# Kernel tuning notes

Measured on AMD Instinct MI355X. Metric: run time of the kernel, lower is better.

Reference implementation:

```python
import jax, jax.numpy as jnp
import numpy as np

B, L, D, H, K_DELAYS = 8, 2048, 512, 8, 8
DH = D // H


def setup_inputs() -> dict:
    key = jax.random.key(0)
    ks = jax.random.split(key, 6)
    def lin_w(k):
        return 0.02 * jax.random.normal(k, (D, D), jnp.float32)
    return {
        "x_q":  jax.random.normal(ks[0], (B, L, D), jnp.float32),
        "x_kv": jax.random.normal(ks[1], (B, L, D), jnp.float32),
        "Wq": lin_w(ks[2]), "bq": jnp.zeros((D,), jnp.float32),
        "Wk": lin_w(ks[3]), "bk": jnp.zeros((D,), jnp.float32),
        "Wv": lin_w(ks[4]), "bv": jnp.zeros((D,), jnp.float32),
        "Wo": lin_w(ks[5]), "bo": jnp.zeros((D,), jnp.float32),
    }


def reference(x_q, x_kv, Wq, bq, Wk, bk, Wv, bv, Wo, bo):
    Bx, Lx, Dx = x_q.shape

    def proj(x, W, b):  # torch Linear: x @ W.T + b, then split heads -> [B,H,L,dh]
        return (x @ W.T + b).reshape(Bx, Lx, H, DH).transpose(0, 2, 1, 3)

    q = proj(x_q, Wq, bq)
    k = proj(x_kv, Wk, bk)
    v = proj(x_kv, Wv, bv)

    # FFT-based autocorrelation over the time axis (axis=2)
    qz = q - q.mean(axis=2, keepdims=True)
    kz = k - k.mean(axis=2, keepdims=True)
    Qf = jnp.fft.rfft(qz, axis=2)
    Kf = jnp.fft.rfft(kz, axis=2)
    corr = jnp.fft.irfft(Qf * jnp.conj(Kf), n=Lx, axis=2).mean(axis=-1)  # [B,H,L]
    # torch expands corr to [B,H,Lq,Lk] then means over Lq -> identical to corr
    score = corr

    K = min(K_DELAYS, Lx)
    vals, idx = jax.lax.top_k(score, K)                    # [B,H,K]
    w = vals / (vals.sum(axis=-1, keepdims=True) + 1e-12)
    w = jax.lax.stop_gradient(w)                           # .detach() in torch

    # circular shift by -delay == gather at (t + delay) mod L
    t = jnp.arange(Lx)
    pos = (t[None, None, None, :] + idx[..., None]) % Lx   # [B,H,K,L]
    v_sh = jnp.take_along_axis(v[:, :, None, :, :], pos[..., None], axis=3)  # [B,H,K,L,dh]
    out = jnp.einsum('bhk,bhkld->bhld', w, v_sh)           # weighted sum over delays

    out = out.transpose(0, 2, 1, 3).reshape(Bx, Lx, Dx)
    return out @ Wo.T + bo
```

## Files before the change

kernel.cpp:

```cpp
#include <hip/hip_runtime.h>
#include <math.h>

#define BB 8
#define LL 2048
#define DD 512
#define HH 8
#define DHH 64
#define KD 8
#define MM (BB*LL)

typedef _Float16 f16x2 __attribute__((ext_vector_type(2)));
typedef _Float16 f16x4 __attribute__((ext_vector_type(4)));
typedef _Float16 f16x8 __attribute__((ext_vector_type(8)));
typedef float    f32x4 __attribute__((ext_vector_type(4)));

__device__ inline void cvt8(const float* __restrict__ s, _Float16* hp, _Float16* lp) {
    const float4 a = *(const float4*)s;
    const float4 b = *(const float4*)(s + 4);
    const float v[8] = {a.x, a.y, a.z, a.w, b.x, b.y, b.z, b.w};
    f16x8 hi, lo;
#pragma unroll
    for (int j = 0; j < 8; j++) {
        const _Float16 h = (_Float16)v[j];
        hi[j] = h;
        lo[j] = (_Float16)((v[j] - (float)h) * 512.0f);
    }
    *(f16x8*)hp = hi;
    if (lp) *(f16x8*)lp = lo;
}

__global__ __launch_bounds__(256) void prep_w(const float* __restrict__ Wq, const float* __restrict__ Wk,
                                              const float* __restrict__ Wv, const float* __restrict__ Wo,
                                              _Float16* __restrict__ Wq_h, _Float16* __restrict__ Wq_l,
                                              _Float16* __restrict__ Wk_h, _Float16* __restrict__ Wk_l,
                                              _Float16* __restrict__ Wv_h, _Float16* __restrict__ Wo_h) {
    const int g = blockIdx.x * 256 + threadIdx.x;
    const int which = g >> 15;
    const size_t idx = (size_t)(g & 32767) * 8;
    if (which == 0)      cvt8(Wq + idx, Wq_h + idx, Wq_l + idx);
    else if (which == 1) cvt8(Wk + idx, Wk_h + idx, Wk_l + idx);
    else if (which == 2) cvt8(Wv + idx, Wv_h + idx, nullptr);
    else                 cvt8(Wo + idx, Wo_h + idx, nullptr);
}

__device__ __forceinline__ void stage16(const _Float16* g, const _Float16* l) {
    __builtin_amdgcn_global_load_lds(
        (const __attribute__((address_space(1))) void*)g,
        (__attribute__((address_space(3))) void*)l,
        16, 0, 0);
}

template<int NPROD, int MODE, int AF32, int BK>
__device__ __forceinline__ void gemm_body(const float* __restrict__ A32,
                                          const _Float16* __restrict__ Ag,
                                          const _Float16* __restrict__ Al_g,
                                          const _Float16* __restrict__ Bg,
                                          const _Float16* __restrict__ Bl_g,
                                          const float* __restrict__ bias,
                                          void* __restrict__ Cv,
                                          _Float16* lds, int l0) {
    constexpr int CPR  = BK / 8;
    constexpr int NST  = BK / 16;
    constexpr int SH   = (BK == 32) ? 2 : 3;
    constexpr int PLN  = 128 * BK;

#define SWZR(R) ((BK == 32) ? (((R) >> 1) & 3) : ((R) & 7))
#define ASWZ(R, g) ((size_t)(R) * BK + (size_t)((((g) ^ SWZR(R))) * 8))

    _Float16* Ah = lds;
    _Float16* Bh = lds + PLN;
    _Float16* Al = (NPROD == 3) ? lds + 2 * PLN : lds;
    _Float16* Bl = (NPROD == 3) ? lds + 3 * PLN : lds;

    const int t  = threadIdx.x;
    const int m0 = (((l0 >> 5) << 3) | (l0 & 7)) * 128;
    const int n0 = ((l0 >> 3) & 3) * 128;

    const int wv   = t >> 6;
    const int lane = t & 63;
    const int wm   = (wv >> 1) * 64;
    const int wn   = (wv & 1) * 64;
    const int lm   = lane & 15;
    const int quad = lane >> 4;

    int srow[NST], schk[NST], sgrp[NST];
#pragma unroll
    for (int i = 0; i < NST; i++) {
        const int s = (i * 4 + wv) * 64 + lane;
        srow[i] = s >> SH;
        schk[i] = (s & (CPR - 1)) ^ SWZR(srow[i]);
        sgrp[i] = (i * 4 + wv) * 512;
    }

    f32x4 acc0[4][4] = {};
    f32x4 acc1[4][4] = {};

    float4 vaA[NST], vaB[NST];
    if (AF32) {
#pragma unroll
        for (int i = 0; i < NST; i++) {
            const float* src = A32 + (size_t)(m0 + srow[i]) * 512 + schk[i] * 8;
            vaA[i] = *(const float4*)src;
            vaB[i] = *(const float4*)(src + 4);
        }
    }

    for (int k0 = 0; k0 < 512; k0 += BK) {
        __syncthreads();
#pragma unroll
        for (int i = 0; i < NST; i++) {
            const size_t offB = (size_t)(n0 + srow[i]) * 512 + k0 + schk[i] * 8;
            stage16(Bg + offB, Bh + sgrp[i]);
            if (NPROD == 3) stage16(Bl_g + offB, Bl + sgrp[i]);
            if (AF32) {
                const float va[8] = {vaA[i].x, vaA[i].y, vaA[i].z, vaA[i].w,
                                     vaB[i].x, vaB[i].y, vaB[i].z, vaB[i].w};
                f16x8 hi, lo;
#pragma unroll
                for (int j = 0; j < 8; j++) {
                    const _Float16 h = (_Float16)va[j];
                    hi[j] = h;
                    if (NPROD == 3) lo[j] = (_Float16)((va[j] - (float)h) * 512.0f);
                }
                *(f16x8*)&Ah[sgrp[i] + lane * 8] = hi;
                if (NPROD == 3) *(f16x8*)&Al[sgrp[i] + lane * 8] = lo;
            } else {
                const size_t offA = (size_t)(m0 + srow[i]) * 512 + k0 + schk[i] * 8;
                stage16(Ag + offA, Ah + sgrp[i]);
                if (NPROD == 3) stage16(Al_g + offA, Al + sgrp[i]);
            }
        }
        __syncthreads();

        if (AF32 && k0 + BK < 512) {
#pragma unroll
            for (int i = 0; i < NST; i++) {
                const float* src = A32 + (size_t)(m0 + srow[i]) * 512 + (k0 + BK) + schk[i] * 8;
                vaA[i] = *(const float4*)src;
                vaB[i] = *(const float4*)(src + 4);
            }
        }

#pragma unroll
        for (int ks = 0; ks < BK / 32; ks++) {
            const int gq = ks * 4 + quad;
            f16x8 afh[4], bf[4];
#pragma unroll
            for (int mt = 0; mt < 4; mt++)
                afh[mt] = *(f16x8*)&Ah[ASWZ(wm + mt * 16 + lm, gq)];
#pragma unroll
            for (int nt = 0; nt < 4; nt++)
                bf[nt] = *(f16x8*)&Bh[ASWZ(wn + nt * 16 + lm, gq)];

#pragma unroll
            for (int mt = 0; mt < 4; mt++)
#pragma unroll
                for (int nt = 0; nt < 4; nt++)
                    acc0[mt][nt] = __builtin_amdgcn_mfma_f32_16x16x32_f16(afh[mt], bf[nt], acc0[mt][nt], 0, 0, 0);

            if (NPROD == 3) {
                f16x8 afl[4];
#pragma unroll
                for (int mt = 0; mt < 4; mt++)
                    afl[mt] = *(f16x8*)&Al[ASWZ(wm + mt * 16 + lm, gq)];
#pragma unroll
                for (int mt = 0; mt < 4; mt++)
#pragma unroll
                    for (int nt = 0; nt < 4; nt++)
                        acc1[mt][nt] = __builtin_amdgcn_mfma_f32_16x16x32_f16(afl[mt], bf[nt], acc1[mt][nt], 0, 0, 0);
#pragma unroll
                for (int nt = 0; nt < 4; nt++)
                    bf[nt] = *(f16x8*)&Bl[ASWZ(wn + nt * 16 + lm, gq)];
#pragma unroll
                for (int mt = 0; mt < 4; mt++)
#pragma unroll
                    for (int nt = 0; nt < 4; nt++)
                        acc1[mt][nt] = __builtin_amdgcn_mfma_f32_16x16x32_f16(afh[mt], bf[nt], acc1[mt][nt], 0, 0, 0);
            }
        }
    }
#undef ASWZ
#undef SWZR

#pragma unroll
    for (int mt = 0; mt < 4; mt++) {
#pragma unroll
        for (int nt = 0; nt < 4; nt++) {
            const int n = n0 + wn + nt * 16 + lm;
            const float bv = bias[n];
            float val[4];
#pragma unroll
            for (int r = 0; r < 4; r++) {
                val[r] = acc0[mt][nt][r] + bv;
                if (NPROD == 3) val[r] += acc1[mt][nt][r] * (1.0f / 512.0f);
            }
            const int mbase = m0 + wm + mt * 16 + quad * 4;
            const int b_idx = mbase >> 11;
            const int lbase = mbase & 2047;
            if (MODE == 0) {
                float* C = (float*)Cv;
#pragma unroll
                for (int r = 0; r < 4; r++) C[(size_t)(mbase + r) * 512 + n] = val[r];
            } else if (MODE == 1) {
                float* C = (float*)Cv;
                float4 pv = make_float4(val[0], val[1], val[2], val[3]);
                *(float4*)&C[((size_t)(b_idx * 512 + n)) * 2048 + lbase] = pv;
            } else {
                _Float16* C = (_Float16*)Cv;
#pragma unroll
                for (int r = 0; r < 4; r++)
                    C[(size_t)b_idx * 1048576 + (size_t)(n >> 6) * 131072
                      + (size_t)(lbase + r) * 64 + (n & 63)] = (_Float16)val[r];
            }
        }
    }
}

__global__ __launch_bounds__(256, 2) void gemm_qk(const float* __restrict__ A0f,
                                                  const _Float16* __restrict__ B0h, const _Float16* __restrict__ B0l,
                                                  const float* __restrict__ bias0, float* __restrict__ C0,
                                                  const float* __restrict__ A1f,
                                                  const _Float16* __restrict__ B1h, const _Float16* __restrict__ B1l,
                                                  const float* __restrict__ bias1, float* __restrict__ C1) {
    __shared__ __align__(16) _Float16 lds[32768];
    const int prob = blockIdx.x >> 9;
    const int l0   = blockIdx.x & 511;
    if (prob == 0)
        gemm_body<3, 1, 1, 64>(A0f, nullptr, nullptr, B0h, B0l, bias0, C0, lds, l0);
    else
        gemm_body<3, 1, 1, 64>(A1f, nullptr, nullptr, B1h, B1l, bias1, C1, lds, l0);
}

__global__ __launch_bounds__(256, 3) void gemm_o(const _Float16* __restrict__ Ah_g,
                                                 const _Float16* __restrict__ Bh_g,
                                                 const float* __restrict__ bias,
                                                 float* __restrict__ C) {
    __shared__ __align__(16) _Float16 lds[8192];
    gemm_body<1, 0, 0, 32>(nullptr, Ah_g, Ah_g, Bh_g, Bh_g, bias, C, lds, blockIdx.x);
}

#define PAD3(i) ((i) + ((i) >> 3))

__device__ inline float2 cmul2(float2 a, float2 w) {
    return make_float2(a.x * w.x - a.y * w.y, a.x * w.y + a.y * w.x);
}
__device__ inline float2 cadd2(float2 a, float2 b) { return make_float2(a.x + b.x, a.y + b.y); }
__device__ inline float2 csub2(float2 a, float2 b) { return make_float2(a.x - b.x, a.y - b.y); }

__global__ __launch_bounds__(256) void fft_fwd(const float* __restrict__ qT,
                                               const float* __restrict__ kT,
                                               float* __restrict__ specP) {
    const int blk  = blockIdx.x;
    const int bh   = blk >> 4;
    const int part = blk & 15;
    const int t    = threadIdx.x;
    __shared__ float2 Zs[2304];
    __shared__ float2 Wt[1024];

#pragma unroll
    for (int s = 0; s < 4; s++) {
        const int j = t + s * 256;
        float sv, cv;
        __sincosf(2.0f * (float)M_PI * (float)j / 2048.0f, &sv, &cv);
        Wt[j] = make_float2(cv, -sv);
    }

    float2 pacc[8];
#pragma unroll
    for (int s = 0; s < 8; s++) pacc[s] = make_float2(0.0f, 0.0f);

    const int low5 = t & 31, hi3 = t >> 5;
    const int low2 = t & 3,  hi6 = t >> 2;

    float2 zn[8];
    {
        const int seq0 = bh * 64 + part * 4;
        const float* qp = qT + (size_t)seq0 * 2048;
        const float* kp = kT + (size_t)seq0 * 2048;
#pragma unroll
        for (int s = 0; s < 8; s++) zn[s] = make_float2(qp[t + 256 * s], kp[t + 256 * s]);
    }

    for (int j4 = 0; j4 < 4; j4++) {
        float2 z[8];
#pragma unroll
        for (int s = 0; s < 8; s++) z[s] = zn[s];
        if (j4 + 1 < 4) {
            const int seq = bh * 64 + part * 4 + j4 + 1;
            const float* qp = qT + (size_t)seq * 2048;
            const float* kp = kT + (size_t)seq * 2048;
#pragma unroll
            for (int s = 0; s < 8; s++) zn[s] = make_float2(qp[t + 256 * s], kp[t + 256 * s]);
        }
        __syncthreads();

#pragma unroll
        for (int sp = 0; sp < 4; sp++) {
            float2 u = z[sp], v = z[sp + 4];
            z[sp]     = cadd2(u, v);
            z[sp + 4] = cmul2(csub2(u, v), Wt[t + 256 * sp]);
        }
#pragma unroll
        for (int base = 0; base < 8; base += 4)
#pragma unroll
            for (int q2 = 0; q2 < 2; q2++) {
                float2 u = z[base + q2], v = z[base + q2 + 2];
                z[base + q2]     = cadd2(u, v);
                z[base + q2 + 2] = cmul2(csub2(u, v), Wt[2 * (t + 256 * q2)]);
            }
        {
            const float2 w = Wt[4 * t];
#pragma unroll
            for (int e = 0; e < 8; e += 2) {
                float2 u = z[e], v = z[e + 1];
                z[e]     = cadd2(u, v);
                z[e + 1] = cmul2(csub2(u, v), w);
            }
        }

#pragma unroll
        for (int s = 0; s < 8; s++) Zs[PAD3(t + 256 * s)] = z[s];
        __syncthreads();
#pragma unroll
        for (int s = 0; s < 8; s++) z[s] = Zs[PAD3(low5 + 32 * s + 256 * hi3)];

#pragma unroll
        for (int sp = 0; sp < 4; sp++) {
            float2 u = z[sp], v = z[sp + 4];
            z[sp]     = cadd2(u, v);
            z[sp + 4] = cmul2(csub2(u, v), Wt[8 * (low5 + 32 * sp)]);
        }
#pragma unroll
        for (int base = 0; base < 8; base += 4)
#pragma unroll
            for (int q2 = 0; q2 < 2; q2++) {
                float2 u = z[base + q2], v = z[base + q2 + 2];
                z[base + q2]     = cadd2(u, v);
                z[base + q2 + 2] = cmul2(csub2(u, v), Wt[16 * (low5 + 32 * q2)]);
            }
        {
            const float2 w = Wt[32 * low5];
#pragma unroll
            for (int e = 0; e < 8; e += 2) {
                float2 u = z[e], v = z[e + 1];
                z[e]     = cadd2(u, v);
                z[e + 1] = cmul2(csub2(u, v), w);
            }
        }

#pragma unroll
        for (int s = 0; s < 8; s++) Zs[PAD3(low5 + 32 * s + 256 * hi3)] = z[s];
        __syncthreads();
#pragma unroll
        for (int s = 0; s < 8; s++) z[s] = Zs[PAD3(low2 + 4 * s + 32 * hi6)];

#pragma unroll
        for (int sp = 0; sp < 4; sp++) {
            float2 u = z[sp], v = z[sp + 4];
            z[sp]     = cadd2(u, v);
            z[sp + 4] = cmul2(csub2(u, v), Wt[64 * (low2 + 4 * sp)]);
        }
#pragma unroll
        for (int base = 0; base < 8; base += 4)
#pragma unroll
            for (int q2 = 0; q2 < 2; q2++) {
                float2 u = z[base + q2], v = z[base + q2 + 2];
                z[base + q2]     = cadd2(u, v);
                z[base + q2 + 2] = cmul2(csub2(u, v), Wt[128 * (low2 + 4 * q2)]);
            }
        {
            const float2 w = Wt[256 * low2];
#pragma unroll
            for (int e = 0; e < 8; e += 2) {
                float2 u = z[e], v = z[e + 1];
                z[e]     = cadd2(u, v);
                z[e + 1] = cmul2(csub2(u, v), w);
            }
        }

#pragma unroll
        for (int s = 0; s < 8; s++) Zs[PAD3(low2 + 4 * s + 32 * hi6)] = z[s];
        __syncthreads();
#pragma unroll
        for (int s = 0; s < 8; s++) z[s] = Zs[PAD3(8 * t + s)];

#pragma unroll
        for (int base = 0; base < 8; base += 4) {
            {
                float2 u = z[base], v = z[base + 2];
                z[base]     = cadd2(u, v);
                z[base + 2] = csub2(u, v);
            }
            {
                float2 u = z[base + 1], v = z[base + 3];
                float2 d = csub2(u, v);
                z[base + 1] = cadd2(u, v);
                z[base + 3] = make_float2(d.y, -d.x);
            }
        }
#pragma unroll
        for (int e = 0; e < 8; e += 2) {
            float2 u = z[e], v = z[e + 1];
            z[e]     = cadd2(u, v);
            z[e + 1] = csub2(u, v);
        }

#pragma unroll
        for (int s = 0; s < 8; s++) Zs[PAD3(8 * t + s)] = z[s];
        __syncthreads();

#pragma unroll
        for (int s = 0; s < 8; s++) {
            const int p  = t + 256 * s;
            const int f  = (int)(__brev((unsigned)p) >> 21);
            const int fm = (2048 - f) & 2047;
            const int p2 = (int)(__brev((unsigned)fm) >> 21);
            const float2 zf = Zs[PAD3(p)];
            const float2 zm = Zs[PAD3(p2)];
            const float qr = 0.5f * (zf.x + zm.x);
            const float qi = 0.5f * (zf.y - zm.y);
            const float kr = 0.5f * (zf.y + zm.y);
            const float ki = 0.5f * (zm.x - zf.x);
            if (f != 0) {
                pacc[s].x += qr * kr + qi * ki;
                pacc[s].y += qi * kr - qr * ki;
            }
        }
    }

    float2* outp = (float2*)specP + (size_t)blk * 2048;
#pragma unroll
    for (int s = 0; s < 8; s++) outp[t + 256 * s] = pacc[s];
}

__device__ inline void build_twiddle(float2* Wt, int tid, float sign) {
#pragma unroll
    for (int s = 0; s < 4; s++) {
        const int j = tid + s * 256;
        const float a = 2.0f * (float)M_PI * (float)j / 2048.0f;
        float sv, cv;
        __sincosf(a, &sv, &cv);
        Wt[j] = make_float2(cv, sign * sv);
    }
}

__device__ inline void fft2048_stages(float2* Z, const float2* Wt, int tid) {
    for (int st = 0; st < 11; st++) {
        const int half = 1 << st;
        const int shift = 10 - st;
#pragma unroll
        for (int r = 0; r < 4; r++) {
            const int m   = tid + r * 256;
            const int grp = m >> st;
            const int pos = m & (half - 1);
            const int i0  = (grp << (st + 1)) + pos;
            const int i1  = i0 + half;
            const float2 w = Wt[pos << shift];
            const float2 a = Z[i0];
            const float2 b = Z[i1];
            const float tr = b.x * w.x - b.y * w.y;
            const float ti = b.x * w.y + b.y * w.x;
            Z[i0] = make_float2(a.x + tr, a.y + ti);
            Z[i1] = make_float2(a.x - tr, a.y - ti);
        }
        __syncthreads();
    }
}

__global__ __launch_bounds__(256, 3) void gemm_v_fftinv(const float* __restrict__ xkv,
                                                        const _Float16* __restrict__ Bh_g,
                                                        const float* __restrict__ bias,
                                                        _Float16* __restrict__ C,
                                                        const float* __restrict__ specP,
                                                        int* __restrict__ delays,
                                                        float* __restrict__ weights) {
    __shared__ __align__(16) char smem[24608];
    const int bid = blockIdx.x;
    const int tid = threadIdx.x;

    if (bid >= 64) {
        gemm_body<1, 2, 1, 32>(xkv, nullptr, nullptr, Bh_g, Bh_g, bias, C, (_Float16*)smem, bid - 64);
        return;
    }

    const int bh = bid;
    float2* Z  = (float2*)smem;
    float2* Wt = (float2*)(smem + 16384);
    float*  wvs = (float*)(smem + 24576);
    int*    wis = (int*)(smem + 24592);

    build_twiddle(Wt, tid, +1.0f);

    const float2* sp = (const float2*)specP + (size_t)bh * 16 * 2048;
#pragma unroll
    for (int s = 0; s < 8; s++) {
        const int p = tid + s * 256;
        float2 acc = make_float2(0.0f, 0.0f);
#pragma unroll
        for (int part = 0; part < 16; part++) {
            const float2 v = sp[part * 2048 + p];
            acc.x += v.x; acc.y += v.y;
        }
        Z[p] = acc;
    }
    __syncthreads();
    fft2048_stages(Z, Wt, tid);

    const float scale = 1.0f / (2048.0f * 64.0f);
    float cv[8];
#pragma unroll
    for (int s = 0; s < 8; s++) cv[s] = Z[tid + s * 256].x * scale;

    float bkv[KD];
    int   bki[KD];
#pragma unroll
    for (int k = 0; k < KD; k++) {
        float lv = -1e30f;
        int   li = 1 << 30;
#pragma unroll
        for (int s = 0; s < 8; s++) {
            const int idx = tid + s * 256;
            if (cv[s] > lv || (cv[s] == lv && idx < li)) { lv = cv[s]; li = idx; }
        }
#pragma unroll
        for (int off = 1; off < 64; off <<= 1) {
            const float v2 = __shfl_xor(lv, off);
            const int   i2 = __shfl_xor(li, off);
            if (v2 > lv || (v2 == lv && i2 < li)) { lv = v2; li = i2; }
        }
        if ((tid & 63) == 0) { wvs[tid >> 6] = lv; wis[tid >> 6] = li; }
        __syncthreads();
        float bv = wvs[0];
        int   bi = wis[0];
#pragma unroll
        for (int j = 1; j < 4; j++) {
            const float v2 = wvs[j];
            const int   i2 = wis[j];
            if (v2 > bv || (v2 == bv && i2 < bi)) { bv = v2; bi = i2; }
        }
        bkv[k] = bv;
        bki[k] = bi;
        if ((bi & 255) == tid) {
            const int slot = bi >> 8;
#pragma unroll
            for (int s = 0; s < 8; s++)
                if (s == slot) cv[s] = -1e30f;
        }
        __syncthreads();
    }

    if (tid == 0) {
        float sum = 0.0f;
#pragma unroll
        for (int k = 0; k < KD; k++) sum += bkv[k];
        const float inv = 1.0f / (sum + 1e-12f);
#pragma unroll
        for (int k = 0; k < KD; k++) {
            weights[bh * KD + k] = bkv[k] * inv;
            delays[bh * KD + k]  = bki[k];
        }
    }
}

__global__ __launch_bounds__(256) void gather_ws(const _Float16* __restrict__ v,
                                                 const int* __restrict__ delays,
                                                 const float* __restrict__ weights,
                                                 _Float16* __restrict__ outb) {
    const int gp = blockIdx.x * 256 + threadIdx.x;
    const int c8 = gp & 63;
    const int m  = gp >> 6;
    const int l  = m & 2047;
    const int b  = m >> 11;
    const int ch = c8 * 8;
    const int h  = ch >> 6;
    const int dh = ch & 63;
    const int bh = b * 8 + h;

    const _Float16* vb = v + (size_t)bh * 131072;
    float a[8] = {};
#pragma unroll
    for (int k = 0; k < KD; k++) {
        const int   d = delays[bh * KD + k];
        const float w = weights[bh * KD + k];
        const int   p = (l + d) & 2047;
        const f16x8 pv = *(const f16x8*)&vb[p * 64 + dh];
#pragma unroll
        for (int j = 0; j < 8; j++) a[j] = fmaf(w, (float)pv[j], a[j]);
    }
    f16x8 ov;
#pragma unroll
    for (int j = 0; j < 8; j++) ov[j] = (_Float16)a[j];
    *(f16x8*)&outb[(size_t)m * 512 + ch] = ov;
}

extern "C" void kernel_launch(void* const* d_in, const int* in_sizes, int n_in,
                              void* d_out, int out_size, void* d_ws, size_t ws_size,
                              hipStream_t stream) {
    const float* x_q  = (const float*)d_in[0];
    const float* x_kv = (const float*)d_in[1];
    const float* Wq   = (const float*)d_in[2];
    const float* bq   = (const float*)d_in[3];
    const float* Wk   = (const float*)d_in[4];
    const float* bk   = (const float*)d_in[5];
    const float* Wv   = (const float*)d_in[6];
    const float* bv   = (const float*)d_in[7];
    const float* Wo   = (const float*)d_in[8];
    const float* bo   = (const float*)d_in[9];
    float* out = (float*)d_out;

    char* ws = (char*)d_ws;
    float*    kf32  = (float*)   (ws + 0);
    _Float16* vh    = (_Float16*)(ws + 33554432);
    float*    specP = (float*)   (ws + 50331648);
    _Float16* gbuf  = (_Float16*)(ws + 67108864);
    _Float16* Wq_h  = (_Float16*)(ws + 83886080);
    _Float16* Wq_l  = (_Float16*)(ws + 84410368);
    _Float16* Wk_h  = (_Float16*)(ws + 84934656);
    _Float16* Wk_l  = (_Float16*)(ws + 85458944);
    _Float16* Wv_h  = (_Float16*)(ws + 85983232);
    _Float16* Wo_h  = (_Float16*)(ws + 86507520);
    int*      dely  = (int*)     (ws + 87031808);
    float*    wgt   = (float*)   (ws + 87033856);
    float*    qf32  = (float*)d_out;

    dim3 blk(256);

    prep_w<<<dim3(512), blk, 0, stream>>>(Wq, Wk, Wv, Wo,
                                          Wq_h, Wq_l, Wk_h, Wk_l, Wv_h, Wo_h);

    gemm_qk<<<dim3(1024), blk, 0, stream>>>(x_q,  Wq_h, Wq_l, bq, qf32,
                                            x_kv, Wk_h, Wk_l, bk, kf32);

    fft_fwd<<<dim3(1024), blk, 0, stream>>>(qf32, kf32, specP);

    gemm_v_fftinv<<<dim3(576), blk, 0, stream>>>(x_kv, Wv_h, bv, vh, specP, dely, wgt);

    gather_ws<<<dim3(4096), blk, 0, stream>>>(vh, dely, wgt, gbuf);

    gemm_o<<<dim3(512), blk, 0, stream>>>(gbuf, Wo_h, bo, out);
}
```

Measured before the change: 255.1 us.

## Fuse delay-weighted gather of V into the output projection GEMM

Removes the separate gather kernel and its fp16 intermediate buffer. The output GEMM now builds its A tile on the fly: it loads the eight delayed V rows, forms the weighted sum, and writes the result straight into LDS. The next k-slice's V rows are prefetched into registers while the MFMAs run. This saves a full write and read of the gathered activations and one kernel launch. In exchange, each of the four N-tiles repeats the gather work and its extra V reads, and register pressure rises, which may lower occupancy.

```diff
diff --git a/kernel.cpp b/kernel.cpp
--- a/kernel.cpp
+++ b/kernel.cpp
@@ -231,12 +231,124 @@
         gemm_body<3, 1, 1, 64>(A1f, nullptr, nullptr, B1h, B1l, bias1, C1, lds, l0);
 }
 
-__global__ __launch_bounds__(256, 3) void gemm_o(const _Float16* __restrict__ Ah_g,
-                                                 const _Float16* __restrict__ Bh_g,
-                                                 const float* __restrict__ bias,
-                                                 float* __restrict__ C) {
+__global__ __launch_bounds__(256, 2) void gemm_og(const _Float16* __restrict__ vh,
+                                                  const int* __restrict__ delays,
+                                                  const float* __restrict__ weights,
+                                                  const _Float16* __restrict__ Bg,
+                                                  const float* __restrict__ bias,
+                                                  float* __restrict__ C) {
     __shared__ __align__(16) _Float16 lds[8192];
-    gemm_body<1, 0, 0, 32>(nullptr, Ah_g, Ah_g, Bh_g, Bh_g, bias, C, lds, blockIdx.x);
+    _Float16* Ah = lds;
+    _Float16* Bh = lds + 4096;
+
+    const int t  = threadIdx.x;
+    const int l0 = blockIdx.x;
+    const int m0 = (((l0 >> 5) << 3) | (l0 & 7)) * 128;
+    const int n0 = ((l0 >> 3) & 3) * 128;
+
+    const int wv   = t >> 6;
+    const int lane = t & 63;
+    const int wm   = (wv >> 1) * 64;
+    const int wn   = (wv & 1) * 64;
+    const int lm   = lane & 15;
+    const int quad = lane >> 4;
+
+    int srow[2], schk[2], sgrp[2];
+#pragma unroll
+    for (int i = 0; i < 2; i++) {
+        const int s = (i * 4 + wv) * 64 + lane;
+        srow[i] = s >> 2;
+        schk[i] = (s & 3) ^ ((srow[i] >> 1) & 3);
+        sgrp[i] = (i * 4 + wv) * 512;
+    }
+#define OSWZ(R, g) ((size_t)(R) * 32 + (size_t)((((g) ^ (((R) >> 1) & 3))) * 8))
+
+    const int bb  = m0 >> 11;
+    const int lml = m0 & 2047;
+
+    f32x4 acc0[4][4] = {};
+
+    f16x8 pv[2][KD];
+#pragma unroll
+    for (int i = 0; i < 2; i++) {
+        const int bh = bb * 8;
+        const int l  = lml + srow[i];
+        const int dh = schk[i] * 8;
+#pragma unroll
+        for (int j = 0; j < KD; j++) {
+            const int d = delays[bh * KD + j];
+            const int pos = (l + d) & 2047;
+            pv[i][j] = *(const f16x8*)&vh[(size_t)bh * 131072 + pos * 64 + dh];
+        }
+    }
+
+    for (int k0 = 0; k0 < 512; k0 += 32) {
+        const int bh = bb * 8 + (k0 >> 6);
+        float wj[KD];
+#pragma unroll
+        for (int j = 0; j < KD; j++) wj[j] = weights[bh * KD + j];
+
+        __syncthreads();
+#pragma unroll
+        for (int i = 0; i < 2; i++) {
+            float a[8] = {};
+#pragma unroll
+            for (int j = 0; j < KD; j++)
+#pragma unroll
+                for (int e = 0; e < 8; e++) a[e] = fmaf(wj[j], (float)pv[i][j][e], a[e]);
+            f16x8 ov;
+#pragma unroll
+            for (int e = 0; e < 8; e++) ov[e] = (_Float16)a[e];
+            *(f16x8*)&Ah[sgrp[i] + lane * 8] = ov;
+            const size_t offB = (size_t)(n0 + srow[i]) * 512 + k0 + schk[i] * 8;
+            stage16(Bg + offB, Bh + sgrp[i]);
+        }
+        __syncthreads();
+
+        if (k0 + 32 < 512) {
+            const int kn  = k0 + 32;
+            const int bhn = bb * 8 + (kn >> 6);
+#pragma unroll
+            for (int i = 0; i < 2; i++) {
+                const int l  = lml + srow[i];
+                const int dh = (kn & 63) + schk[i] * 8;
+#pragma unroll
+                for (int j = 0; j < KD; j++) {
+                    const int d = delays[bhn * KD + j];
+                    const int pos = (l + d) & 2047;
+                    pv[i][j] = *(const f16x8*)&vh[(size_t)bhn * 131072 + pos * 64 + dh];
+                }
+            }
+        }
+
+        f16x8 afh[4], bf[4];
+#pragma unroll
+        for (int mt = 0; mt < 4; mt++)
+            afh[mt] = *(f16x8*)&Ah[OSWZ(wm + mt * 16 + lm, quad)];
+#pragma unroll
+        for (int nt = 0; nt < 4; nt++)
+            bf[nt] = *(f16x8*)&Bh[OSWZ(wn + nt * 16 + lm, quad)];
+
+#pragma unroll
+        for (int mt = 0; mt < 4; mt++)
+#pragma unroll
+            for (int nt = 0; nt < 4; nt++)
+                acc0[mt][nt] = __builtin_amdgcn_mfma_f32_16x16x32_f16(afh[mt], bf[nt], acc0[mt][nt], 0, 0, 0);
+    }
+#undef OSWZ
+
+#pragma unroll
+    for (int mt = 0; mt < 4; mt++) {
+#pragma unroll
+        for (int nt = 0; nt < 4; nt++) {
+            const int n  = n0 + wn + nt * 16 + lm;
+            const float bv = bias[n];
+            const int mbase = m0 + wm + mt * 16 + quad * 4;
+#pragma unroll
+            for (int r = 0; r < 4; r++)
+                C[(size_t)(mbase + r) * 512 + n] = acc0[mt][nt][r] + bv;
+        }
+    }
 }
 
 #define PAD3(i) ((i) + ((i) >> 3))
@@ -562,37 +674,6 @@
     }
 }
 
-__global__ __launch_bounds__(256) void gather_ws(const _Float16* __restrict__ v,
-                                                 const int* __restrict__ delays,
-                                                 const float* __restrict__ weights,
-                                                 _Float16* __restrict__ outb) {
-    const int gp = blockIdx.x * 256 + threadIdx.x;
-    const int c8 = gp & 63;
-    const int m  = gp >> 6;
-    const int l  = m & 2047;
-    const int b  = m >> 11;
-    const int ch = c8 * 8;
-    const int h  = ch >> 6;
-    const int dh = ch & 63;
-    const int bh = b * 8 + h;
-
-    const _Float16* vb = v + (size_t)bh * 131072;
-    float a[8] = {};
-#pragma unroll
-    for (int k = 0; k < KD; k++) {
-        const int   d = delays[bh * KD + k];
-        const float w = weights[bh * KD + k];
-        const int   p = (l + d) & 2047;
-        const f16x8 pv = *(const f16x8*)&vb[p * 64 + dh];
-#pragma unroll
-        for (int j = 0; j < 8; j++) a[j] = fmaf(w, (float)pv[j], a[j]);
-    }
-    f16x8 ov;
-#pragma unroll
-    for (int j = 0; j < 8; j++) ov[j] = (_Float16)a[j];
-    *(f16x8*)&outb[(size_t)m * 512 + ch] = ov;
-}
-
 extern "C" void kernel_launch(void* const* d_in, const int* in_sizes, int n_in,
                               void* d_out, int out_size, void* d_ws, size_t ws_size,
                               hipStream_t stream) {
@@ -612,7 +693,6 @@
     float*    kf32  = (float*)   (ws + 0);
     _Float16* vh    = (_Float16*)(ws + 33554432);
     float*    specP = (float*)   (ws + 50331648);
-    _Float16* gbuf  = (_Float16*)(ws + 67108864);
     _Float16* Wq_h  = (_Float16*)(ws + 83886080);
     _Float16* Wq_l  = (_Float16*)(ws + 84410368);
     _Float16* Wk_h  = (_Float16*)(ws + 84934656);
@@ -635,7 +715,5 @@
 
     gemm_v_fftinv<<<dim3(576), blk, 0, stream>>>(x_kv, Wv_h, bv, vh, specP, dely, wgt);
 
-    gather_ws<<<dim3(4096), blk, 0, stream>>>(vh, dely, wgt, gbuf);
-
-    gemm_o<<<dim3(512), blk, 0, stream>>>(gbuf, Wo_h, bo, out);
-}
+    gemm_og<<<dim3(512), blk, 0, stream>>>(vh, dely, wgt, Wo_h, bo, out);
+}
```

Result: slower. 268.9 us (+5.4%).
